# Performance work log

Measured on AMD Instinct MI355X. Metric: run time of the kernel, lower is better.

## Reference

```python
import jax, jax.numpy as jnp
import numpy as np

N_BINS = 15
N = 16777216
NUM_CLASSES = 1000


def setup_inputs() -> dict:
    key = jax.random.key(0)
    k1, k2, k3 = jax.random.split(key, 3)
    confidences = jax.random.uniform(k1, (N,), dtype=jnp.float32)
    predictions = jax.random.randint(k2, (N,), 0, NUM_CLASSES, dtype=jnp.int32)
    labels = jax.random.randint(k3, (N,), 0, NUM_CLASSES, dtype=jnp.int32)
    return {"confidences": confidences, "predictions": predictions, "labels": labels}


def reference(confidences, predictions, labels):
    # Bin i covers (b[i], b[i+1]] exactly as torch's gt(lower) & le(upper).
    boundaries = jnp.linspace(0.0, 1.0, N_BINS + 1)
    # side='left': first idx with boundaries[idx] >= conf, so conf in (b[k], b[k+1]] -> bin k.
    bin_ids = jnp.searchsorted(boundaries, confidences, side='left') - 1
    valid = (bin_ids >= 0) & (bin_ids < N_BINS)  # conf <= 0 falls in no bin
    ids = jnp.clip(bin_ids, 0, N_BINS - 1)
    w = valid.astype(confidences.dtype)

    acc = (predictions == labels).astype(confidences.dtype)
    counts = jax.ops.segment_sum(w, ids, num_segments=N_BINS)
    conf_sum = jax.ops.segment_sum(confidences * w, ids, num_segments=N_BINS)
    acc_sum = jax.ops.segment_sum(acc * w, ids, num_segments=N_BINS)

    n_total = confidences.shape[0]
    nonempty = counts > 0
    denom = jnp.where(nonempty, counts, 1.0)
    avg_conf = conf_sum / denom
    avg_acc = acc_sum / denom
    prop = counts / n_total
    ece = jnp.sum(jnp.where(nonempty, jnp.abs(avg_conf - avg_acc) * prop, 0.0))
    return ece.reshape(1)
```

## Files before the change

kernel.cpp:

```cpp
#include <hip/hip_runtime.h>

#define NBINS 15
#define NREP 8
#define REP_STRIDE 16
#define WS_WORDS (NREP * REP_STRIDE)


__global__ void ece_init(float* __restrict__ ws) {
    int t = threadIdx.x;
    if (t < WS_WORDS) ws[t] = 0.0f;
}

#define ECE_ELEM(cv_, pr_, lb_)                                                 \
    do {                                                                        \
        float cv = (cv_);                                                       \
        int b = (int)ceilf(cv * 15.0f) - 1;                                     \
        float d = cv - (((pr_) == (lb_)) ? 1.0f : 0.0f);                        \
        d = ((unsigned)b < 15u) ? d : 0.0f;                \
        a0  += (b == 0)  ? d : 0.0f;  a1  += (b == 1)  ? d : 0.0f;              \
        a2  += (b == 2)  ? d : 0.0f;  a3  += (b == 3)  ? d : 0.0f;              \
        a4  += (b == 4)  ? d : 0.0f;  a5  += (b == 5)  ? d : 0.0f;              \
        a6  += (b == 6)  ? d : 0.0f;  a7  += (b == 7)  ? d : 0.0f;              \
        a8  += (b == 8)  ? d : 0.0f;  a9  += (b == 9)  ? d : 0.0f;              \
        a10 += (b == 10) ? d : 0.0f;  a11 += (b == 11) ? d : 0.0f;              \
        a12 += (b == 12) ? d : 0.0f;  a13 += (b == 13) ? d : 0.0f;              \
        a14 += (b == 14) ? d : 0.0f;                                            \
    } while (0)

#define WAVE_RED(A)                                                             \
    do {                                                                        \
        A += __shfl_xor(A, 1, 64);  A += __shfl_xor(A, 2, 64);                  \
        A += __shfl_xor(A, 4, 64);  A += __shfl_xor(A, 8, 64);                  \
        A += __shfl_xor(A, 16, 64); A += __shfl_xor(A, 32, 64);                 \
    } while (0)

__global__ __launch_bounds__(256) void ece_main(const float* __restrict__ conf,
                                                const int* __restrict__ pred,
                                                const int* __restrict__ lab,
                                                float* __restrict__ ws,
                                                int nvec) {
    float a0 = 0.0f, a1 = 0.0f, a2 = 0.0f, a3 = 0.0f, a4 = 0.0f;
    float a5 = 0.0f, a6 = 0.0f, a7 = 0.0f, a8 = 0.0f, a9 = 0.0f;
    float a10 = 0.0f, a11 = 0.0f, a12 = 0.0f, a13 = 0.0f, a14 = 0.0f;

    const float4* __restrict__ c4 = (const float4*)conf;
    const int4*   __restrict__ p4 = (const int4*)pred;
    const int4*   __restrict__ l4 = (const int4*)lab;

    int tid    = blockIdx.x * blockDim.x + threadIdx.x;
    int stride = gridDim.x * blockDim.x;

    int i = tid;
    for (; i + stride < nvec; i += 2 * stride) {
        float4 c0 = c4[i];
        float4 c1 = c4[i + stride];
        int4   p0 = p4[i];
        int4   p1 = p4[i + stride];
        int4   l0 = l4[i];
        int4   l1 = l4[i + stride];

        ECE_ELEM(c0.x, p0.x, l0.x); ECE_ELEM(c0.y, p0.y, l0.y);
        ECE_ELEM(c0.z, p0.z, l0.z); ECE_ELEM(c0.w, p0.w, l0.w);
        ECE_ELEM(c1.x, p1.x, l1.x); ECE_ELEM(c1.y, p1.y, l1.y);
        ECE_ELEM(c1.z, p1.z, l1.z); ECE_ELEM(c1.w, p1.w, l1.w);
    }
    for (; i < nvec; i += stride) {
        float4 c = c4[i];
        int4   p = p4[i];
        int4   l = l4[i];
        ECE_ELEM(c.x, p.x, l.x); ECE_ELEM(c.y, p.y, l.y);
        ECE_ELEM(c.z, p.z, l.z); ECE_ELEM(c.w, p.w, l.w);
    }

    WAVE_RED(a0);  WAVE_RED(a1);  WAVE_RED(a2);  WAVE_RED(a3);  WAVE_RED(a4);
    WAVE_RED(a5);  WAVE_RED(a6);  WAVE_RED(a7);  WAVE_RED(a8);  WAVE_RED(a9);
    WAVE_RED(a10); WAVE_RED(a11); WAVE_RED(a12); WAVE_RED(a13); WAVE_RED(a14);

    __shared__ float s_h[4][16];
    int wave = threadIdx.x >> 6;
    int lane = threadIdx.x & 63;
    if (lane == 0) {
        s_h[wave][0]  = a0;  s_h[wave][1]  = a1;  s_h[wave][2]  = a2;
        s_h[wave][3]  = a3;  s_h[wave][4]  = a4;  s_h[wave][5]  = a5;
        s_h[wave][6]  = a6;  s_h[wave][7]  = a7;  s_h[wave][8]  = a8;
        s_h[wave][9]  = a9;  s_h[wave][10] = a10; s_h[wave][11] = a11;
        s_h[wave][12] = a12; s_h[wave][13] = a13; s_h[wave][14] = a14;
    }
    __syncthreads();
    if (threadIdx.x < NBINS) {
        int k = threadIdx.x;
        float s = s_h[0][k] + s_h[1][k] + s_h[2][k] + s_h[3][k];
        atomicAdd(ws + (blockIdx.x & (NREP - 1)) * REP_STRIDE + k, s);
    }
}

__global__ void ece_final(const float* __restrict__ ws, float* __restrict__ out,
                          float inv_n) {
    int k = threadIdx.x;
    float v = 0.0f;
    if (k < NBINS) {
        float s = 0.0f;
#pragma unroll
        for (int r = 0; r < NREP; ++r) s += ws[r * REP_STRIDE + k];
        v = fabsf(s) * inv_n;
    }
    WAVE_RED(v);
    if (k == 0) out[0] = v;
}

extern "C" void kernel_launch(void* const* d_in, const int* in_sizes, int n_in,
                              void* d_out, int out_size, void* d_ws, size_t ws_size,
                              hipStream_t stream) {
    const float* conf = (const float*)d_in[0];
    const int*   pred = (const int*)d_in[1];
    const int*   lab  = (const int*)d_in[2];
    float* ws  = (float*)d_ws;
    float* out = (float*)d_out;
    int n    = in_sizes[0];
    int nvec = n / 4;

    ece_init<<<1, 128, 0, stream>>>(ws);
    ece_main<<<2048, 256, 0, stream>>>(conf, pred, lab, ws, nvec);
    ece_final<<<1, 64, 0, stream>>>(ws, out, 1.0f / (float)n);
}
```

Before: 46.24 us.

## Use per-lane shared-memory histograms and per-block partials instead of register bins

Replaces the 15 predicated register accumulators per element with a single LDS atomicAdd into a per-wave, per-lane histogram. It also drops the init kernel and global atomics: each block writes its partial sums to the workspace and a wider final kernel reduces them. The aim is to cut ALU work per element and remove one launch. In exchange it adds LDS atomics on the hot path, a 16KB shared allocation and an extra barrier, and the final kernel must now read 2048x15 partials.

```diff
diff --git a/kernel.cpp b/kernel.cpp
--- a/kernel.cpp
+++ b/kernel.cpp
@@ -1,31 +1,6 @@
 #include <hip/hip_runtime.h>
 
 #define NBINS 15
-#define NREP 8
-#define REP_STRIDE 16
-#define WS_WORDS (NREP * REP_STRIDE)
-
-
-__global__ void ece_init(float* __restrict__ ws) {
-    int t = threadIdx.x;
-    if (t < WS_WORDS) ws[t] = 0.0f;
-}
-
-#define ECE_ELEM(cv_, pr_, lb_)                                                 \
-    do {                                                                        \
-        float cv = (cv_);                                                       \
-        int b = (int)ceilf(cv * 15.0f) - 1;                                     \
-        float d = cv - (((pr_) == (lb_)) ? 1.0f : 0.0f);                        \
-        d = ((unsigned)b < 15u) ? d : 0.0f;                \
-        a0  += (b == 0)  ? d : 0.0f;  a1  += (b == 1)  ? d : 0.0f;              \
-        a2  += (b == 2)  ? d : 0.0f;  a3  += (b == 3)  ? d : 0.0f;              \
-        a4  += (b == 4)  ? d : 0.0f;  a5  += (b == 5)  ? d : 0.0f;              \
-        a6  += (b == 6)  ? d : 0.0f;  a7  += (b == 7)  ? d : 0.0f;              \
-        a8  += (b == 8)  ? d : 0.0f;  a9  += (b == 9)  ? d : 0.0f;              \
-        a10 += (b == 10) ? d : 0.0f;  a11 += (b == 11) ? d : 0.0f;              \
-        a12 += (b == 12) ? d : 0.0f;  a13 += (b == 13) ? d : 0.0f;              \
-        a14 += (b == 14) ? d : 0.0f;                                            \
-    } while (0)
 
 #define WAVE_RED(A)                                                             \
     do {                                                                        \
@@ -34,14 +9,33 @@
         A += __shfl_xor(A, 16, 64); A += __shfl_xor(A, 32, 64);                 \
     } while (0)
 
+#define ECE_ELEM(cv_, pr_, lb_)                                                 \
+    do {                                                                        \
+        float cv = (cv_);                                                       \
+        int b = (int)ceilf(cv * 15.0f) - 1;                                     \
+        float d = cv - (((pr_) == (lb_)) ? 1.0f : 0.0f);                        \
+        bool ok = ((unsigned)b < 15u);                     \
+        d = ok ? d : 0.0f;                                                      \
+        b = ok ? b : 0;                                                         \
+        atomicAdd(&hist[wave][b][lane], d);                                     \
+    } while (0)
+
 __global__ __launch_bounds__(256) void ece_main(const float* __restrict__ conf,
                                                 const int* __restrict__ pred,
                                                 const int* __restrict__ lab,
                                                 float* __restrict__ ws,
                                                 int nvec) {
-    float a0 = 0.0f, a1 = 0.0f, a2 = 0.0f, a3 = 0.0f, a4 = 0.0f;
-    float a5 = 0.0f, a6 = 0.0f, a7 = 0.0f, a8 = 0.0f, a9 = 0.0f;
-    float a10 = 0.0f, a11 = 0.0f, a12 = 0.0f, a13 = 0.0f, a14 = 0.0f;
+    __shared__ float hist[4][16][64];
+    __shared__ float s_blk[4][16];
+
+    int wave = threadIdx.x >> 6;
+    int lane = threadIdx.x & 63;
+
+    {
+        float* h = &hist[0][0][0];
+        for (int j = threadIdx.x; j < 4 * 16 * 64; j += 256) h[j] = 0.0f;
+    }
+    __syncthreads();
 
     const float4* __restrict__ c4 = (const float4*)conf;
     const int4*   __restrict__ p4 = (const int4*)pred;
@@ -72,40 +66,41 @@
         ECE_ELEM(c.z, p.z, l.z); ECE_ELEM(c.w, p.w, l.w);
     }
 
-    WAVE_RED(a0);  WAVE_RED(a1);  WAVE_RED(a2);  WAVE_RED(a3);  WAVE_RED(a4);
-    WAVE_RED(a5);  WAVE_RED(a6);  WAVE_RED(a7);  WAVE_RED(a8);  WAVE_RED(a9);
-    WAVE_RED(a10); WAVE_RED(a11); WAVE_RED(a12); WAVE_RED(a13); WAVE_RED(a14);
-
-    __shared__ float s_h[4][16];
-    int wave = threadIdx.x >> 6;
-    int lane = threadIdx.x & 63;
-    if (lane == 0) {
-        s_h[wave][0]  = a0;  s_h[wave][1]  = a1;  s_h[wave][2]  = a2;
-        s_h[wave][3]  = a3;  s_h[wave][4]  = a4;  s_h[wave][5]  = a5;
-        s_h[wave][6]  = a6;  s_h[wave][7]  = a7;  s_h[wave][8]  = a8;
-        s_h[wave][9]  = a9;  s_h[wave][10] = a10; s_h[wave][11] = a11;
-        s_h[wave][12] = a12; s_h[wave][13] = a13; s_h[wave][14] = a14;
+#pragma unroll
+    for (int k = 0; k < NBINS; ++k) {
+        float f = hist[wave][k][lane];
+        WAVE_RED(f);
+        if (lane == 0) s_blk[wave][k] = f;
     }
     __syncthreads();
+
     if (threadIdx.x < NBINS) {
         int k = threadIdx.x;
-        float s = s_h[0][k] + s_h[1][k] + s_h[2][k] + s_h[3][k];
-        atomicAdd(ws + (blockIdx.x & (NREP - 1)) * REP_STRIDE + k, s);
+        ws[blockIdx.x * 16 + k] =
+            s_blk[0][k] + s_blk[1][k] + s_blk[2][k] + s_blk[3][k];
     }
 }
 
-__global__ void ece_final(const float* __restrict__ ws, float* __restrict__ out,
-                          float inv_n) {
-    int k = threadIdx.x;
+__global__ __launch_bounds__(256) void ece_final(const float* __restrict__ ws,
+                                                 float* __restrict__ out,
+                                                 float inv_n, int nblocks) {
+    __shared__ float s_f[16];
+    int t   = threadIdx.x;
+    int bin = t >> 4;
+    int idx = t & 15;
+    float p = 0.0f;
+    if (t < 240) {
+        for (int j = idx; j < nblocks; j += 16) p += ws[j * 16 + bin];
+    }
+    p += __shfl_xor(p, 1, 64); p += __shfl_xor(p, 2, 64);
+    p += __shfl_xor(p, 4, 64); p += __shfl_xor(p, 8, 64);
+    if (t < 240 && idx == 0) s_f[bin] = p;
+    __syncthreads();
+
     float v = 0.0f;
-    if (k < NBINS) {
-        float s = 0.0f;
-#pragma unroll
-        for (int r = 0; r < NREP; ++r) s += ws[r * REP_STRIDE + k];
-        v = fabsf(s) * inv_n;
-    }
+    if (t < NBINS) v = fabsf(s_f[t]) * inv_n;
     WAVE_RED(v);
-    if (k == 0) out[0] = v;
+    if (t == 0) out[0] = v;
 }
 
 extern "C" void kernel_launch(void* const* d_in, const int* in_sizes, int n_in,
@@ -119,7 +114,13 @@
     int n    = in_sizes[0];
     int nvec = n / 4;
 
-    ece_init<<<1, 128, 0, stream>>>(ws);
-    ece_main<<<2048, 256, 0, stream>>>(conf, pred, lab, ws, nvec);
-    ece_final<<<1, 64, 0, stream>>>(ws, out, 1.0f / (float)n);
+    int nblocks = 2048;
+    size_t need = (size_t)nblocks * 16 * sizeof(float);
+    if (ws_size < need) {
+        nblocks = (int)(ws_size / (16 * sizeof(float)));
+        if (nblocks < 1) nblocks = 1;
+    }
+
+    ece_main<<<nblocks, 256, 0, stream>>>(conf, pred, lab, ws, nvec);
+    ece_final<<<1, 256, 0, stream>>>(ws, out, 1.0f / (float)n, nblocks);
 }
```

New measurement: 135.5 us. +193.0%, slower.

## Replace atomics with per-block partials, drop init kernel, software-pipeline loads

Applied to the files above, without the earlier changes.

Removes the zero-init kernel launch by having each block write its per-bin partial sums to a dedicated workspace slot, and the final kernel now reduces 2048 partials per bin in parallel. The main loop becomes a software-pipelined single-stride loop that prefetches the next iteration's loads while computing the current one, with a launch-bounds occupancy hint. This trades one launch and global atomics for a larger final reduction and a different load schedule. The loop issues one extra redundant load on its last iteration.

```diff
diff --git a/kernel.cpp b/kernel.cpp
--- a/kernel.cpp
+++ b/kernel.cpp
@@ -1,15 +1,14 @@
 #include <hip/hip_runtime.h>
 
 #define NBINS 15
-#define NREP 8
-#define REP_STRIDE 16
-#define WS_WORDS (NREP * REP_STRIDE)
+#define NBLK  2048
 
-
-__global__ void ece_init(float* __restrict__ ws) {
-    int t = threadIdx.x;
-    if (t < WS_WORDS) ws[t] = 0.0f;
-}
+#define WAVE_RED(A)                                                             \
+    do {                                                                        \
+        A += __shfl_xor(A, 1, 64);  A += __shfl_xor(A, 2, 64);                  \
+        A += __shfl_xor(A, 4, 64);  A += __shfl_xor(A, 8, 64);                  \
+        A += __shfl_xor(A, 16, 64); A += __shfl_xor(A, 32, 64);                 \
+    } while (0)
 
 #define ECE_ELEM(cv_, pr_, lb_)                                                 \
     do {                                                                        \
@@ -27,18 +26,11 @@
         a14 += (b == 14) ? d : 0.0f;                                            \
     } while (0)
 
-#define WAVE_RED(A)                                                             \
-    do {                                                                        \
-        A += __shfl_xor(A, 1, 64);  A += __shfl_xor(A, 2, 64);                  \
-        A += __shfl_xor(A, 4, 64);  A += __shfl_xor(A, 8, 64);                  \
-        A += __shfl_xor(A, 16, 64); A += __shfl_xor(A, 32, 64);                 \
-    } while (0)
-
-__global__ __launch_bounds__(256) void ece_main(const float* __restrict__ conf,
-                                                const int* __restrict__ pred,
-                                                const int* __restrict__ lab,
-                                                float* __restrict__ ws,
-                                                int nvec) {
+__global__ __launch_bounds__(256, 8) void ece_main(const float* __restrict__ conf,
+                                                   const int* __restrict__ pred,
+                                                   const int* __restrict__ lab,
+                                                   float* __restrict__ ws,
+                                                   int nvec) {
     float a0 = 0.0f, a1 = 0.0f, a2 = 0.0f, a3 = 0.0f, a4 = 0.0f;
     float a5 = 0.0f, a6 = 0.0f, a7 = 0.0f, a8 = 0.0f, a9 = 0.0f;
     float a10 = 0.0f, a11 = 0.0f, a12 = 0.0f, a13 = 0.0f, a14 = 0.0f;
@@ -47,27 +39,32 @@
     const int4*   __restrict__ p4 = (const int4*)pred;
     const int4*   __restrict__ l4 = (const int4*)lab;
 
-    int tid    = blockIdx.x * blockDim.x + threadIdx.x;
-    int stride = gridDim.x * blockDim.x;
+    const int tid    = blockIdx.x * blockDim.x + threadIdx.x;
+    const int stride = gridDim.x * blockDim.x;
+    const int niter  = nvec / stride;
 
     int i = tid;
-    for (; i + stride < nvec; i += 2 * stride) {
-        float4 c0 = c4[i];
-        float4 c1 = c4[i + stride];
-        int4   p0 = p4[i];
-        int4   p1 = p4[i + stride];
-        int4   l0 = l4[i];
-        int4   l1 = l4[i + stride];
+    float4 cc = c4[i];
+    int4   pc = p4[i];
+    int4   lc = l4[i];
 
-        ECE_ELEM(c0.x, p0.x, l0.x); ECE_ELEM(c0.y, p0.y, l0.y);
-        ECE_ELEM(c0.z, p0.z, l0.z); ECE_ELEM(c0.w, p0.w, l0.w);
-        ECE_ELEM(c1.x, p1.x, l1.x); ECE_ELEM(c1.y, p1.y, l1.y);
-        ECE_ELEM(c1.z, p1.z, l1.z); ECE_ELEM(c1.w, p1.w, l1.w);
+    for (int it = 0; it < niter; ++it) {
+        int inext = i + stride;
+        int j = (it + 1 < niter) ? inext : tid;
+        float4 cn = c4[j];
+        int4   pn = p4[j];
+        int4   ln = l4[j];
+
+        ECE_ELEM(cc.x, pc.x, lc.x); ECE_ELEM(cc.y, pc.y, lc.y);
+        ECE_ELEM(cc.z, pc.z, lc.z); ECE_ELEM(cc.w, pc.w, lc.w);
+
+        cc = cn; pc = pn; lc = ln;
+        i = inext;
     }
-    for (; i < nvec; i += stride) {
-        float4 c = c4[i];
-        int4   p = p4[i];
-        int4   l = l4[i];
+    for (int r = tid + niter * stride; r < nvec; r += stride) {
+        float4 c = c4[r];
+        int4   p = p4[r];
+        int4   l = l4[r];
         ECE_ELEM(c.x, p.x, l.x); ECE_ELEM(c.y, p.y, l.y);
         ECE_ELEM(c.z, p.z, l.z); ECE_ELEM(c.w, p.w, l.w);
     }
@@ -89,23 +86,32 @@
     __syncthreads();
     if (threadIdx.x < NBINS) {
         int k = threadIdx.x;
-        float s = s_h[0][k] + s_h[1][k] + s_h[2][k] + s_h[3][k];
-        atomicAdd(ws + (blockIdx.x & (NREP - 1)) * REP_STRIDE + k, s);
+        ws[k * NBLK + blockIdx.x] =
+            s_h[0][k] + s_h[1][k] + s_h[2][k] + s_h[3][k];
     }
 }
 
-__global__ void ece_final(const float* __restrict__ ws, float* __restrict__ out,
-                          float inv_n) {
-    int k = threadIdx.x;
+__global__ __launch_bounds__(256) void ece_final(const float* __restrict__ ws,
+                                                 float* __restrict__ out,
+                                                 float inv_n) {
+    __shared__ float s_f[16];
+    int t   = threadIdx.x;
+    int bin = t >> 4;
+    int idx = t & 15;
+    float p = 0.0f;
+    if (t < 240) {
+        const float* row = ws + bin * NBLK;
+        for (int j = idx; j < NBLK; j += 16) p += row[j];
+    }
+    p += __shfl_xor(p, 1, 64); p += __shfl_xor(p, 2, 64);
+    p += __shfl_xor(p, 4, 64); p += __shfl_xor(p, 8, 64);
+    if (t < 240 && idx == 0) s_f[bin] = p;
+    __syncthreads();
+
     float v = 0.0f;
-    if (k < NBINS) {
-        float s = 0.0f;
-#pragma unroll
-        for (int r = 0; r < NREP; ++r) s += ws[r * REP_STRIDE + k];
-        v = fabsf(s) * inv_n;
-    }
+    if (t < NBINS) v = fabsf(s_f[t]) * inv_n;
     WAVE_RED(v);
-    if (k == 0) out[0] = v;
+    if (t == 0) out[0] = v;
 }
 
 extern "C" void kernel_launch(void* const* d_in, const int* in_sizes, int n_in,
@@ -119,7 +125,6 @@
     int n    = in_sizes[0];
     int nvec = n / 4;
 
-    ece_init<<<1, 128, 0, stream>>>(ws);
-    ece_main<<<2048, 256, 0, stream>>>(conf, pred, lab, ws, nvec);
-    ece_final<<<1, 64, 0, stream>>>(ws, out, 1.0f / (float)n);
+    ece_main<<<NBLK, 256, 0, stream>>>(conf, pred, lab, ws, nvec);
+    ece_final<<<1, 256, 0, stream>>>(ws, out, 1.0f / (float)n);
 }
```

Measured after the change: 63.46 us. 37.2% more time.
